# Kernel tuning notes

Hardware: AMD Instinct MI355X
Metric: run time of the kernel (lower is better)

Reference implementation:

```python
import jax, jax.numpy as jnp
import numpy as np

B, S, E, H = 2, 2048, 1024, 16
D = E // H  # head dimension = 64


def setup_inputs() -> dict:
    key = jax.random.key(0)
    ks = jax.random.split(key, 12)
    scale_in = 1.0 / np.sqrt(E)
    x = jax.random.normal(ks[0], (B, S, E), dtype=jnp.float32)
    # random 0/1 attention mask (1 = attend, 0 = masked out)
    mask = jax.random.randint(ks[1], (B, S, S), 0, 2, dtype=jnp.int32)
    # per-head QKV projections, stacked over the head axis: [H, E, D]
    Wq = jax.random.normal(ks[2], (H, E, D), dtype=jnp.float32) * scale_in
    bq = jnp.zeros((H, D), dtype=jnp.float32)
    Wk = jax.random.normal(ks[3], (H, E, D), dtype=jnp.float32) * scale_in
    bk = jnp.zeros((H, D), dtype=jnp.float32)
    Wv = jax.random.normal(ks[4], (H, E, D), dtype=jnp.float32) * scale_in
    bv = jnp.zeros((H, D), dtype=jnp.float32)
    # output projection: [H*D, E] == [E, E]
    Wo = jax.random.normal(ks[5], (H * D, E), dtype=jnp.float32) * scale_in
    bo = jnp.zeros((E,), dtype=jnp.float32)
    return {"x": x, "mask": mask, "Wq": Wq, "bq": bq, "Wk": Wk, "bk": bk,
            "Wv": Wv, "bv": bv, "Wo": Wo, "bo": bo}


def reference(x, mask, Wq, bq, Wk, bk, Wv, bv, Wo, bo):
    # Batched equivalent of the per-head Python loop: all heads at once.
    q = jnp.einsum('bse,hed->bhsd', x, Wq) + bq[None, :, None, :]  # [B,H,S,D]
    k = jnp.einsum('bse,hed->bhsd', x, Wk) + bk[None, :, None, :]
    v = jnp.einsum('bse,hed->bhsd', x, Wv) + bv[None, :, None, :]
    scale = 1.0 / jnp.sqrt(jnp.asarray(D, dtype=q.dtype))
    scores = jnp.einsum('bhsd,bhtd->bhst', q, k) * scale          # [B,H,S,S]
    scores = jnp.where(mask[:, None, :, :] != 0, scores, jnp.asarray(-1e9, scores.dtype))
    attn = jax.nn.softmax(scores, axis=-1)
    ctx = jnp.einsum('bhst,bhtd->bhsd', attn, v)                  # [B,H,S,D]
    # concat heads along feature dim (torch.cat(dim=2))
    concat = jnp.transpose(ctx, (0, 2, 1, 3)).reshape(B, S, H * D)
    return concat @ Wo + bo
```

## Files before the change

kernel.cpp:

```cpp
#include <hip/hip_runtime.h>

#define S_LEN 2048
#define EMB   1024
#define NH    16
#define HD    64
#define BS    2
#define QSCALE 0.18033688f

typedef __bf16 bf16;
typedef bf16  bf16x8 __attribute__((ext_vector_type(8)));
typedef bf16  bf16x4 __attribute__((ext_vector_type(4)));
typedef float f32x4  __attribute__((ext_vector_type(4)));
typedef unsigned long long u64;
typedef unsigned int u32;

__device__ __forceinline__ bf16x8 ld8(const bf16* p){ return *(const bf16x8*)p; }

__device__ __forceinline__ void gl_lds16(const bf16* g, void* l) {
    __builtin_amdgcn_global_load_lds(
        (const __attribute__((address_space(1))) void*)g,
        (__attribute__((address_space(3))) void*)l,
        16, 0, 0);
}

#define SW(row, g) ((((g) ^ ((row) & 7))) * 8)

__global__ __launch_bounds__(256)
void pack_mask(const int* __restrict__ mask, u64* __restrict__ pm)
{
    int lane = threadIdx.x & 63;
    int row  = blockIdx.x * 4 + (threadIdx.x >> 6);
    const int* mr = mask + (size_t)row * S_LEN;
    u64* pr = pm + (size_t)row * (S_LEN / 64);
    for (int i = 0; i < S_LEN / 64; ++i) {
        u64 bits = __ballot(mr[i * 64 + lane] != 0);
        if (lane == 0) pr[i] = bits;
    }
}

__global__ __launch_bounds__(256)
void transpose_w(const float* __restrict__ W0, const float* __restrict__ W1,
                 const float* __restrict__ W2, const float* __restrict__ W3,
                 bf16* __restrict__ Wt)
{
    const int z = blockIdx.z;
    const float* W = z == 0 ? W0 : z == 1 ? W1 : z == 2 ? W2 : W3;
    const bool head = z < 3;
    const int k0 = blockIdx.x * 64, n0 = blockIdx.y * 64;
    const int tid = threadIdx.x;
    __shared__ float T[64][68];
    {
        int k = k0 + (tid >> 2), cg = (tid & 3) * 16;
        size_t base = head ? ((size_t)(n0 >> 6) * ((size_t)EMB * HD) + (size_t)k * HD + cg)
                           : ((size_t)k * EMB + n0 + cg);
        #pragma unroll
        for (int g = 0; g < 4; ++g) {
            f32x4 v = *(const f32x4*)(W + base + g * 4);
            #pragma unroll
            for (int j = 0; j < 4; ++j) T[tid >> 2][cg + g * 4 + j] = v[j];
        }
    }
    __syncthreads();
    {
        int n = n0 + (tid >> 2), ck = (tid & 3) * 16;
        bf16 t16[16];
        #pragma unroll
        for (int j = 0; j < 16; ++j) t16[j] = (bf16)T[ck + j][tid >> 2];
        bf16* outp = Wt + (size_t)z * EMB * EMB + (size_t)n * EMB + k0 + ck;
        *(bf16x8*)outp       = *(bf16x8*)t16;
        *(bf16x8*)(outp + 8) = *(bf16x8*)(t16 + 8);
    }
}

__global__ __launch_bounds__(256)
void cvt_f32_bf16(const float* __restrict__ x, bf16* __restrict__ y)
{
    size_t i = ((size_t)blockIdx.x * 256 + threadIdx.x) * 16;
    bf16 t[16];
    #pragma unroll
    for (int g = 0; g < 4; ++g) {
        f32x4 v = *(const f32x4*)(x + i + g * 4);
        #pragma unroll
        for (int j = 0; j < 4; ++j) t[g * 4 + j] = (bf16)v[j];
    }
    *(bf16x8*)(y + i)     = *(bf16x8*)t;
    *(bf16x8*)(y + i + 8) = *(bf16x8*)(t + 8);
}

__global__ __launch_bounds__(256)
void scale_q(bf16* __restrict__ q)
{
    size_t i = ((size_t)blockIdx.x * 256 + threadIdx.x) * 8;
    bf16x8 v = *(bf16x8*)(q + i);
    #pragma unroll
    for (int j = 0; j < 8; ++j) v[j] = (bf16)((float)v[j] * QSCALE);
    *(bf16x8*)(q + i) = v;
}

__global__ __launch_bounds__(256, 3)
void gemm_qkv(const void* __restrict__ Ap, const bf16* __restrict__ Wt,
              const float* __restrict__ bqp, const float* __restrict__ bkp,
              const float* __restrict__ bvp,
              bf16* __restrict__ qb, bf16* __restrict__ kb, bf16* __restrict__ VT,
              int a32)
{
    const int tid  = threadIdx.x;
    const int lane = tid & 63, quad = lane >> 4, c = lane & 15;
    const int w = tid >> 6, wm = w >> 1, wn = w & 1;
    const int m0 = blockIdx.x * 128;
    const int n0 = blockIdx.y * 128;

    __shared__ bf16 Ash[128][64];
    __shared__ bf16 Wsh[128][64];

    f32x4 acc[4][4];
    #pragma unroll
    for (int mt = 0; mt < 4; ++mt)
        #pragma unroll
        for (int nt = 0; nt < 4; ++nt) acc[mt][nt] = (f32x4){0.f,0.f,0.f,0.f};

    const int lrow = lane >> 3, lcol = (lane & 7) * 8;

    for (int k0 = 0; k0 < EMB; k0 += 64) {
        __syncthreads();
        if (!a32) {
            const bf16* A = (const bf16*)Ap;
            #pragma unroll
            for (int j = 0; j < 4; ++j)
                gl_lds16(A + (size_t)(m0 + w * 32 + j * 8 + lrow) * EMB + k0 + lcol,
                         &Ash[w * 32 + j * 8][0]);
        } else {
            const float* A = (const float*)Ap + (size_t)(m0 + (tid >> 1)) * EMB + k0 + (tid & 1) * 32;
            bf16 t[32];
            #pragma unroll
            for (int g = 0; g < 8; ++g) {
                f32x4 v = *(const f32x4*)(A + g * 4);
                #pragma unroll
                for (int j = 0; j < 4; ++j) t[g * 4 + j] = (bf16)v[j];
            }
            #pragma unroll
            for (int g2 = 0; g2 < 4; ++g2)
                *(bf16x8*)&Ash[tid >> 1][(tid & 1) * 32 + g2 * 8] = *(bf16x8*)(t + g2 * 8);
        }
        #pragma unroll
        for (int j = 0; j < 4; ++j)
            gl_lds16(Wt + (size_t)(n0 + w * 32 + j * 8 + lrow) * EMB + k0 + lcol,
                     &Wsh[w * 32 + j * 8][0]);
        __syncthreads();

        #pragma unroll
        for (int kh = 0; kh < 2; ++kh) {
            bf16x8 af[4], bfv[4];
            #pragma unroll
            for (int mt = 0; mt < 4; ++mt) af[mt]  = ld8(&Ash[wm * 64 + mt * 16 + c][kh * 32 + quad * 8]);
            #pragma unroll
            for (int nt = 0; nt < 4; ++nt) bfv[nt] = ld8(&Wsh[wn * 64 + nt * 16 + c][kh * 32 + quad * 8]);
            #pragma unroll
            for (int mt = 0; mt < 4; ++mt)
                #pragma unroll
                for (int nt = 0; nt < 4; ++nt)
                    acc[mt][nt] = __builtin_amdgcn_mfma_f32_16x16x32_bf16(af[mt], bfv[nt], acc[mt][nt], 0, 0, 0);
        }
    }

    const int z = n0 >> 10;
    const float* bias = z == 0 ? bqp : z == 1 ? bkp : bvp;
    #pragma unroll
    for (int nt = 0; nt < 4; ++nt) {
        int nn = (n0 & 1023) + wn * 64 + nt * 16 + c;
        float bv_ = bias[nn];
        #pragma unroll
        for (int mt = 0; mt < 4; ++mt)
            #pragma unroll
            for (int r = 0; r < 4; ++r) {
                int m = m0 + wm * 64 + mt * 16 + quad * 4 + r;
                float v = acc[mt][nt][r] + bv_;
                if (z == 0)      qb[(size_t)m * EMB + nn] = (bf16)(v * QSCALE);
                else if (z == 1) kb[(size_t)m * EMB + nn] = (bf16)v;
                else {
                    int head = nn >> 6, d = nn & 63;
                    VT[((size_t)((m >> 11) * NH + head) * HD + d) * S_LEN + (m & 2047)] = (bf16)v;
                }
            }
    }
}

__global__ __launch_bounds__(256, 3)
void gemm_o(const bf16* __restrict__ Ap, const bf16* __restrict__ Wt,
            const float* __restrict__ bo, float* __restrict__ C)
{
    const int tid  = threadIdx.x;
    const int lane = tid & 63, quad = lane >> 4, c = lane & 15;
    const int w = tid >> 6, wm = w >> 1, wn = w & 1;
    const int m0 = blockIdx.x * 128;
    const int n0 = blockIdx.y * 128;

    __shared__ bf16 Ash[128][64];
    __shared__ bf16 Wsh[128][64];

    f32x4 acc[4][4];
    #pragma unroll
    for (int mt = 0; mt < 4; ++mt)
        #pragma unroll
        for (int nt = 0; nt < 4; ++nt) acc[mt][nt] = (f32x4){0.f,0.f,0.f,0.f};

    const int lrow = lane >> 3, lcol = (lane & 7) * 8;

    for (int k0 = 0; k0 < EMB; k0 += 64) {
        __syncthreads();
        #pragma unroll
        for (int j = 0; j < 4; ++j)
            gl_lds16(Ap + (size_t)(m0 + w * 32 + j * 8 + lrow) * EMB + k0 + lcol,
                     &Ash[w * 32 + j * 8][0]);
        #pragma unroll
        for (int j = 0; j < 4; ++j)
            gl_lds16(Wt + (size_t)(n0 + w * 32 + j * 8 + lrow) * EMB + k0 + lcol,
                     &Wsh[w * 32 + j * 8][0]);
        __syncthreads();

        #pragma unroll
        for (int kh = 0; kh < 2; ++kh) {
            bf16x8 af[4], bfv[4];
            #pragma unroll
            for (int mt = 0; mt < 4; ++mt) af[mt]  = ld8(&Ash[wm * 64 + mt * 16 + c][kh * 32 + quad * 8]);
            #pragma unroll
            for (int nt = 0; nt < 4; ++nt) bfv[nt] = ld8(&Wsh[wn * 64 + nt * 16 + c][kh * 32 + quad * 8]);
            #pragma unroll
            for (int mt = 0; mt < 4; ++mt)
                #pragma unroll
                for (int nt = 0; nt < 4; ++nt)
                    acc[mt][nt] = __builtin_amdgcn_mfma_f32_16x16x32_bf16(af[mt], bfv[nt], acc[mt][nt], 0, 0, 0);
        }
    }

    #pragma unroll
    for (int nt = 0; nt < 4; ++nt) {
        int n = n0 + wn * 64 + nt * 16 + c;
        float bv_ = bo[n];
        #pragma unroll
        for (int mt = 0; mt < 4; ++mt)
            #pragma unroll
            for (int r = 0; r < 4; ++r) {
                int m = m0 + wm * 64 + mt * 16 + quad * 4 + r;
                C[(size_t)m * EMB + n] = acc[mt][nt][r] + bv_;
            }
    }
}

__global__ __launch_bounds__(512)
void gemm128(const void* __restrict__ Ap, const float* __restrict__ Wp,
             const bf16* __restrict__ Wtp, const float* __restrict__ bias,
             void* __restrict__ Cp, int N, int K, int whead,
             int m_base, int a32, int cmode)
{
    const int tid  = threadIdx.x;
    const int lane = tid & 63, quad = lane >> 4, c = lane & 15;
    const int w = tid >> 6, wm = w >> 2, wn = w & 3;
    const int m0 = blockIdx.x * 128, n0 = blockIdx.y * 128;

    __shared__ bf16 Ash[128][64];
    __shared__ bf16 Wsh[128][64];

    f32x4 acc[4][2];
    #pragma unroll
    for (int mt = 0; mt < 4; ++mt)
        #pragma unroll
        for (int nt = 0; nt < 2; ++nt) acc[mt][nt] = (f32x4){0.f,0.f,0.f,0.f};

    const int arow = tid >> 2, aq = tid & 3;

    auto compute = [&]() {
        #pragma unroll
        for (int kh = 0; kh < 2; ++kh) {
            bf16x8 bfr[2];
            #pragma unroll
            for (int nt = 0; nt < 2; ++nt) {
                int rw = wn * 32 + nt * 16 + c;
                bfr[nt] = ld8(&Wsh[rw][SW(rw, kh * 4 + quad)]);
            }
            #pragma unroll
            for (int mt = 0; mt < 4; ++mt) {
                int ra = wm * 64 + mt * 16 + c;
                bf16x8 af = ld8(&Ash[ra][SW(ra, kh * 4 + quad)]);
                #pragma unroll
                for (int nt = 0; nt < 2; ++nt)
                    acc[mt][nt] = __builtin_amdgcn_mfma_f32_16x16x32_bf16(af, bfr[nt], acc[mt][nt], 0, 0, 0);
            }
        }
    };

    for (int k0 = 0; k0 < K; k0 += 64) {
        __syncthreads();
        if (a32) {
            const float* A = (const float*)Ap + (size_t)(m_base + m0 + arow) * K + k0 + aq * 16;
            bf16 t16[16];
            #pragma unroll
            for (int g = 0; g < 4; ++g) {
                f32x4 v = *(const f32x4*)(A + g * 4);
                #pragma unroll
                for (int j = 0; j < 4; ++j) t16[g * 4 + j] = (bf16)v[j];
            }
            *(bf16x8*)&Ash[arow][SW(arow, aq * 2)]     = *(bf16x8*)t16;
            *(bf16x8*)&Ash[arow][SW(arow, aq * 2 + 1)] = *(bf16x8*)(t16 + 8);
        } else {
            const bf16* A = (const bf16*)Ap + (size_t)(m_base + m0 + arow) * K + k0 + aq * 16;
            *(bf16x8*)&Ash[arow][SW(arow, aq * 2)]     = ld8(A);
            *(bf16x8*)&Ash[arow][SW(arow, aq * 2 + 1)] = ld8(A + 8);
        }
        {
            int nl = tid & 127, kg = tid >> 7;
            int n = n0 + nl;
            size_t base    = whead ? ((size_t)(n >> 6) * ((size_t)K * HD) + (n & 63))
                                   : (size_t)n;
            size_t kstride = whead ? (size_t)HD : (size_t)N;
            #pragma unroll
            for (int p = 0; p < 2; ++p) {
                int grp = kg + 4 * p;
                bf16 t8[8];
                #pragma unroll
                for (int j = 0; j < 8; ++j)
                    t8[j] = (bf16)Wp[base + (size_t)(k0 + grp * 8 + j) * kstride];
                *(bf16x8*)&Wsh[nl][SW(nl, grp)] = *(bf16x8*)t8;
            }
        }
        __syncthreads();
        compute();
    }

    #pragma unroll
    for (int nt = 0; nt < 2; ++nt) {
        int n = n0 + wn * 32 + nt * 16 + c;
        float bv_ = bias[n];
        #pragma unroll
        for (int mt = 0; mt < 4; ++mt)
            #pragma unroll
            for (int r = 0; r < 4; ++r) {
                int m = m0 + wm * 64 + mt * 16 + quad * 4 + r;
                float v = acc[mt][nt][r] + bv_;
                if (cmode == 0)      ((bf16*)Cp)[(size_t)m * N + n] = (bf16)v;
                else if (cmode == 1) ((float*)Cp)[(size_t)m * N + n] = v;
                else {
                    int mm = m_base + m;
                    ((bf16*)Cp)[((size_t)((mm >> 11) * NH + (n >> 6)) * HD + (n & 63)) * S_LEN + (mm & 2047)] = (bf16)v;
                }
            }
    }
}

__global__ __launch_bounds__(512, 2)
void attn_kernel(bf16* q0p, bf16* q1p, const bf16* __restrict__ kbuf,
                 const bf16* __restrict__ VTg, const u64* __restrict__ pmask)
{
    const int tid  = threadIdx.x;
    const int w    = tid >> 6;
    const int lane = tid & 63;
    const int quad = lane >> 4;
    const int c    = lane & 15;
    const int flat  = blockIdx.y * 16 + blockIdx.x;
    const int flat2 = (flat & 7) * 64 + (flat >> 3);
    const int q0   = (flat2 & 15) * 128;
    const int bh   = flat2 >> 4;
    const int b    = bh >> 4, h = bh & 15;

    bf16* qc = b ? q1p : q0p;
    const bf16* kh_ = kbuf + (size_t)b * S_LEN * EMB + h * HD;
    const bf16* vt  = VTg + (size_t)bh * HD * S_LEN;

    __shared__ bf16 Ksh [2][64][64];
    __shared__ bf16 VTsh[2][64][64];
    __shared__ bf16 Psh[8][16][64];

    bf16x8 qf[2];
    #pragma unroll
    for (int kk = 0; kk < 2; ++kk)
        qf[kk] = ld8(qc + (size_t)(q0 + w * 16 + c) * EMB + h * HD + kk * 32 + quad * 8);

    const u64* pmr = pmask + (size_t)(b * S_LEN + q0 + w * 16 + c) * (S_LEN / 64);

    f32x4 l4 = (f32x4){0.f,0.f,0.f,0.f};
    f32x4 o[4];
    #pragma unroll
    for (int dt = 0; dt < 4; ++dt) o[dt] = (f32x4){0.f,0.f,0.f,0.f};

    const int srow = tid >> 3, sg = tid & 7;
    bf16x8 kr, vr;
    auto loadKV = [&](int t0) {
        kr = ld8(kh_ + (size_t)(t0 + srow) * EMB + sg * 8);
        vr = ld8(vt + (size_t)srow * S_LEN + t0 + sg * 8);
    };

    loadKV(0);
    int buf = 0;
    for (int t0 = 0; t0 < S_LEN; t0 += 64) {
        *(bf16x8*)&Ksh [buf][srow][SW(srow, sg)] = kr;
        *(bf16x8*)&VTsh[buf][srow][SW(srow, sg)] = vr;
        __syncthreads();
        if (t0 + 64 < S_LEN) loadKV(t0 + 64);

        u64 s0 = pmr[t0 >> 6] >> (quad * 4);
        u32 mm[2] = {(u32)s0, (u32)(s0 >> 32)};

        f32x4 sc[4];
        #pragma unroll
        for (int tt = 0; tt < 4; ++tt) sc[tt] = (f32x4){0.f,0.f,0.f,0.f};
        #pragma unroll
        for (int tt = 0; tt < 4; ++tt)
            #pragma unroll
            for (int kk = 0; kk < 2; ++kk) {
                int rk = tt * 16 + c;
                bf16x8 ka = ld8(&Ksh[buf][rk][SW(rk, kk * 4 + quad)]);
                sc[tt] = __builtin_amdgcn_mfma_f32_16x16x32_bf16(ka, qf[kk], sc[tt], 0, 0, 0);
            }

        #pragma unroll
        for (int tt = 0; tt < 4; ++tt) {
            u32 half = mm[tt >> 1];
            bf16x4 pv;
            #pragma unroll
            for (int r = 0; r < 4; ++r) {
                float e = __builtin_amdgcn_exp2f(sc[tt][r]);
                e = ((half >> ((tt & 1) * 16 + r)) & 1) ? e : 0.f;
                l4[r] += e;
                pv[r] = (bf16)e;
            }
            *(bf16x4*)&Psh[w][c][SW(c, tt * 2 + (quad >> 1)) + (quad & 1) * 4] = pv;
        }
        __builtin_amdgcn_s_waitcnt(0xc07f);

        #pragma unroll
        for (int th = 0; th < 2; ++th) {
            bf16x8 pf = ld8(&Psh[w][c][SW(c, th * 4 + quad)]);
            #pragma unroll
            for (int dt = 0; dt < 4; ++dt) {
                int rv = dt * 16 + c;
                bf16x8 av = ld8(&VTsh[buf][rv][SW(rv, th * 4 + quad)]);
                o[dt] = __builtin_amdgcn_mfma_f32_16x16x32_bf16(av, pf, o[dt], 0, 0, 0);
            }
        }
        buf ^= 1;
    }

    float ls = l4[0] + l4[1] + l4[2] + l4[3];
    ls += __shfl_xor(ls, 16);
    ls += __shfl_xor(ls, 32);
    float inv = 1.0f / fmaxf(ls, 1e-30f);
    #pragma unroll
    for (int dt = 0; dt < 4; ++dt) {
        bf16x4 ov;
        #pragma unroll
        for (int r = 0; r < 4; ++r) ov[r] = (bf16)(o[dt][r] * inv);
        *(bf16x4*)&qc[(size_t)(q0 + w * 16 + c) * EMB + h * HD + dt * 16 + quad * 4] = ov;
    }
}

extern "C" void kernel_launch(void* const* d_in, const int* in_sizes, int n_in,
                              void* d_out, int out_size, void* d_ws, size_t ws_size,
                              hipStream_t stream)
{
    const float* x    = (const float*)d_in[0];
    const int*   mask = (const int*)d_in[1];
    const float* Wq   = (const float*)d_in[2];
    const float* bq   = (const float*)d_in[3];
    const float* Wk   = (const float*)d_in[4];
    const float* bk   = (const float*)d_in[5];
    const float* Wv   = (const float*)d_in[6];
    const float* bv   = (const float*)d_in[7];
    const float* Wo   = (const float*)d_in[8];
    const float* bo   = (const float*)d_in[9];
    float* out = (float*)d_out;

    const size_t SLAB = (size_t)S_LEN * EMB;
    const size_t QB = (size_t)BS * SLAB * sizeof(bf16);
    const size_t WT = (size_t)4 * EMB * EMB * sizeof(bf16);
    const size_t PM = (size_t)BS * S_LEN * (S_LEN / 64) * 8;
    const size_t XB = (size_t)BS * SLAB * sizeof(bf16);

    bf16* VT = (bf16*)d_out;
    bf16* kb = (bf16*)d_out + BS * SLAB;

    dim3 b256(256), b512(512);
    dim3 gAtt (S_LEN / 128, BS * NH);
    dim3 gT   (EMB / 64, EMB / 64, 4);
    dim3 gPk  (BS * S_LEN / 4);
    dim3 gFull(BS * S_LEN / 128, EMB / 128);
    dim3 gHalf(S_LEN / 128, EMB / 128);

    if (ws_size >= QB + WT + PM + 64) {
        bf16* qb  = (bf16*)d_ws;
        bf16* Wt  = (bf16*)((char*)d_ws + QB);
        u64*  pm  = (u64*)((char*)d_ws + QB + WT);
        const void* xA = x; int a32 = 1;
        if (ws_size >= QB + WT + PM + XB + 64) {
            bf16* xbf = (bf16*)((char*)d_ws + QB + WT + PM);
            cvt_f32_bf16<<<dim3(1024), b256, 0, stream>>>(x, xbf);
            xA = xbf; a32 = 0;
        }
        pack_mask<<<gPk, b256, 0, stream>>>(mask, pm);
        transpose_w<<<gT, b256, 0, stream>>>(Wq, Wk, Wv, Wo, Wt);

        gemm_qkv<<<dim3(BS * S_LEN / 128, 3 * EMB / 128), b256, 0, stream>>>(
            xA, Wt, bq, bk, bv, qb, kb, VT, a32);

        attn_kernel<<<gAtt, b512, 0, stream>>>(qb, qb + SLAB, kb, VT, pm);

        gemm_o<<<dim3(BS * S_LEN / 128, EMB / 128), b256, 0, stream>>>(
            qb, Wt + (size_t)3 * EMB * EMB, bo, out);
    } else if (ws_size >= QB + PM + 64) {
        bf16* qb = (bf16*)d_ws;
        u64*  pm = (u64*)((char*)d_ws + QB);
        pack_mask<<<gPk, b256, 0, stream>>>(mask, pm);

        gemm128<<<gFull, b512, 0, stream>>>(x, Wk, nullptr, bk, kb, EMB, EMB, 1, 0, 1, 0);
        gemm128<<<gFull, b512, 0, stream>>>(x, Wv, nullptr, bv, VT, EMB, EMB, 1, 0, 1, 2);
        gemm128<<<gFull, b512, 0, stream>>>(x, Wq, nullptr, bq, qb, EMB, EMB, 1, 0, 1, 0);
        scale_q<<<dim3(BS * SLAB / (256 * 8)), b256, 0, stream>>>(qb);

        attn_kernel<<<gAtt, b512, 0, stream>>>(qb, qb + SLAB, kb, VT, pm);

        gemm128<<<gFull, b512, 0, stream>>>(qb, Wo, nullptr, bo, out, EMB, EMB, 0, 0, 0, 1);
    } else {
        bf16* qb0 = (bf16*)d_in[4];
        bf16* qb1 = (bf16*)d_in[6];
        u64*  pm  = (u64*)d_in[2];

        gemm128<<<gFull, b512, 0, stream>>>(x, Wk, nullptr, bk, kb, EMB, EMB, 1, 0, 1, 0);
        gemm128<<<gFull, b512, 0, stream>>>(x, Wv, nullptr, bv, VT, EMB, EMB, 1, 0, 1, 2);
        gemm128<<<gHalf, b512, 0, stream>>>(x, Wq, nullptr, bq, qb0, EMB, EMB, 1, 0,     1, 0);
        gemm128<<<gHalf, b512, 0, stream>>>(x, Wq, nullptr, bq, qb1, EMB, EMB, 1, S_LEN, 1, 0);
        scale_q<<<dim3(SLAB / (256 * 8)), b256, 0, stream>>>(qb0);
        scale_q<<<dim3(SLAB / (256 * 8)), b256, 0, stream>>>(qb1);
        pack_mask<<<gPk, b256, 0, stream>>>(mask, pm);

        attn_kernel<<<gAtt, b512, 0, stream>>>(qb0, qb1, kb, VT, pm);

        gemm128<<<gHalf, b512, 0, stream>>>(qb0, Wo, nullptr, bo, out,        EMB, EMB, 0, 0, 0, 1);
        gemm128<<<gHalf, b512, 0, stream>>>(qb1, Wo, nullptr, bo, out + SLAB, EMB, EMB, 0, 0, 0, 1);
    }
}
```

Baseline: 244.1 us.

## Split attention warps 4x2 over query and key/dim halves for operand reuse

Reorganizes the attention kernel's 8 warps into a 4x2 grid. Each warp handles 32 query rows and half of the 64-key tile for QK^T, and half of the head dimension for PV. Each K and V fragment loaded from LDS now feeds two MFMAs, which halves LDS reads per MFMA. In exchange, P is shared through LDS across warps, so each tile needs an extra __syncthreads, and row sums are combined through LDS at the end.

Measured after the change: 245.4 us. Within noise of the previous version (+0.5%).

```diff
diff --git a/kernel.cpp b/kernel.cpp
--- a/kernel.cpp
+++ b/kernel.cpp
@@ -356,6 +356,8 @@
     const int lane = tid & 63;
     const int quad = lane >> 4;
     const int c    = lane & 15;
+    const int qw   = w & 3;
+    const int kw   = w >> 2;
     const int flat  = blockIdx.y * 16 + blockIdx.x;
     const int flat2 = (flat & 7) * 64 + (flat >> 3);
     const int q0   = (flat2 & 15) * 128;
@@ -368,19 +370,25 @@
 
     __shared__ bf16 Ksh [2][64][64];
     __shared__ bf16 VTsh[2][64][64];
-    __shared__ bf16 Psh[8][16][64];
-
-    bf16x8 qf[2];
-    #pragma unroll
-    for (int kk = 0; kk < 2; ++kk)
-        qf[kk] = ld8(qc + (size_t)(q0 + w * 16 + c) * EMB + h * HD + kk * 32 + quad * 8);
-
-    const u64* pmr = pmask + (size_t)(b * S_LEN + q0 + w * 16 + c) * (S_LEN / 64);
-
-    f32x4 l4 = (f32x4){0.f,0.f,0.f,0.f};
-    f32x4 o[4];
-    #pragma unroll
-    for (int dt = 0; dt < 4; ++dt) o[dt] = (f32x4){0.f,0.f,0.f,0.f};
+    __shared__ bf16 Psh[128][64];
+    __shared__ float Lsh[2][4][2][16];
+
+    bf16x8 qf[2][2];
+    #pragma unroll
+    for (int rq = 0; rq < 2; ++rq)
+        #pragma unroll
+        for (int kk = 0; kk < 2; ++kk)
+            qf[rq][kk] = ld8(qc + (size_t)(q0 + qw * 32 + rq * 16 + c) * EMB + h * HD + kk * 32 + quad * 8);
+
+    const u64* pmr0 = pmask + (size_t)(b * S_LEN + q0 + qw * 32 + c) * (S_LEN / 64);
+    const u64* pmr1 = pmr0 + (size_t)16 * (S_LEN / 64);
+
+    float l2[2] = {0.f, 0.f};
+    f32x4 o[2][2];
+    #pragma unroll
+    for (int dt = 0; dt < 2; ++dt)
+        #pragma unroll
+        for (int rq = 0; rq < 2; ++rq) o[dt][rq] = (f32x4){0.f,0.f,0.f,0.f};
 
     const int srow = tid >> 3, sg = tid & 7;
     bf16x8 kr, vr;
@@ -395,61 +403,92 @@
         *(bf16x8*)&Ksh [buf][srow][SW(srow, sg)] = kr;
         *(bf16x8*)&VTsh[buf][srow][SW(srow, sg)] = vr;
         __syncthreads();
+
+        u64 pm0 = pmr0[t0 >> 6], pm1 = pmr1[t0 >> 6];
+        u32 h0 = (u32)(pm0 >> (kw * 32 + quad * 4));
+        u32 h1 = (u32)(pm1 >> (kw * 32 + quad * 4));
+
+        f32x4 sc[2][2];
+        #pragma unroll
+        for (int tt = 0; tt < 2; ++tt)
+            #pragma unroll
+            for (int rq = 0; rq < 2; ++rq) sc[tt][rq] = (f32x4){0.f,0.f,0.f,0.f};
+        #pragma unroll
+        for (int tt = 0; tt < 2; ++tt)
+            #pragma unroll
+            for (int kk = 0; kk < 2; ++kk) {
+                int rk = kw * 32 + tt * 16 + c;
+                bf16x8 ka = ld8(&Ksh[buf][rk][SW(rk, kk * 4 + quad)]);
+                #pragma unroll
+                for (int rq = 0; rq < 2; ++rq)
+                    sc[tt][rq] = __builtin_amdgcn_mfma_f32_16x16x32_bf16(ka, qf[rq][kk], sc[tt][rq], 0, 0, 0);
+            }
+
+        #pragma unroll
+        for (int rq = 0; rq < 2; ++rq) {
+            u32 hh = rq ? h1 : h0;
+            int q = qw * 32 + rq * 16 + c;
+            #pragma unroll
+            for (int tt = 0; tt < 2; ++tt) {
+                bf16x4 pv;
+                #pragma unroll
+                for (int r = 0; r < 4; ++r) {
+                    float e = __builtin_amdgcn_exp2f(sc[tt][rq][r]);
+                    e = ((hh >> (tt * 16 + r)) & 1) ? e : 0.f;
+                    l2[rq] += e;
+                    pv[r] = (bf16)e;
+                }
+                *(bf16x4*)&Psh[q][SW(q, kw * 4 + tt * 2 + (quad >> 1)) + (quad & 1) * 4] = pv;
+            }
+        }
+        __syncthreads();
+
         if (t0 + 64 < S_LEN) loadKV(t0 + 64);
 
-        u64 s0 = pmr[t0 >> 6] >> (quad * 4);
-        u32 mm[2] = {(u32)s0, (u32)(s0 >> 32)};
-
-        f32x4 sc[4];
-        #pragma unroll
-        for (int tt = 0; tt < 4; ++tt) sc[tt] = (f32x4){0.f,0.f,0.f,0.f};
-        #pragma unroll
-        for (int tt = 0; tt < 4; ++tt)
-            #pragma unroll
-            for (int kk = 0; kk < 2; ++kk) {
-                int rk = tt * 16 + c;
-                bf16x8 ka = ld8(&Ksh[buf][rk][SW(rk, kk * 4 + quad)]);
-                sc[tt] = __builtin_amdgcn_mfma_f32_16x16x32_bf16(ka, qf[kk], sc[tt], 0, 0, 0);
-            }
-
-        #pragma unroll
-        for (int tt = 0; tt < 4; ++tt) {
-            u32 half = mm[tt >> 1];
-            bf16x4 pv;
-            #pragma unroll
-            for (int r = 0; r < 4; ++r) {
-                float e = __builtin_amdgcn_exp2f(sc[tt][r]);
-                e = ((half >> ((tt & 1) * 16 + r)) & 1) ? e : 0.f;
-                l4[r] += e;
-                pv[r] = (bf16)e;
-            }
-            *(bf16x4*)&Psh[w][c][SW(c, tt * 2 + (quad >> 1)) + (quad & 1) * 4] = pv;
-        }
-        __builtin_amdgcn_s_waitcnt(0xc07f);
-
         #pragma unroll
         for (int th = 0; th < 2; ++th) {
-            bf16x8 pf = ld8(&Psh[w][c][SW(c, th * 4 + quad)]);
-            #pragma unroll
-            for (int dt = 0; dt < 4; ++dt) {
-                int rv = dt * 16 + c;
+            bf16x8 pf[2];
+            #pragma unroll
+            for (int rq = 0; rq < 2; ++rq) {
+                int q = qw * 32 + rq * 16 + c;
+                pf[rq] = ld8(&Psh[q][SW(q, th * 4 + quad)]);
+            }
+            #pragma unroll
+            for (int dt = 0; dt < 2; ++dt) {
+                int rv = kw * 32 + dt * 16 + c;
                 bf16x8 av = ld8(&VTsh[buf][rv][SW(rv, th * 4 + quad)]);
-                o[dt] = __builtin_amdgcn_mfma_f32_16x16x32_bf16(av, pf, o[dt], 0, 0, 0);
+                #pragma unroll
+                for (int rq = 0; rq < 2; ++rq)
+                    o[dt][rq] = __builtin_amdgcn_mfma_f32_16x16x32_bf16(av, pf[rq], o[dt][rq], 0, 0, 0);
             }
         }
         buf ^= 1;
     }
 
-    float ls = l4[0] + l4[1] + l4[2] + l4[3];
-    ls += __shfl_xor(ls, 16);
-    ls += __shfl_xor(ls, 32);
-    float inv = 1.0f / fmaxf(ls, 1e-30f);
-    #pragma unroll
-    for (int dt = 0; dt < 4; ++dt) {
-        bf16x4 ov;
-        #pragma unroll
-        for (int r = 0; r < 4; ++r) ov[r] = (bf16)(o[dt][r] * inv);
-        *(bf16x4*)&qc[(size_t)(q0 + w * 16 + c) * EMB + h * HD + dt * 16 + quad * 4] = ov;
+    float lr[2];
+    #pragma unroll
+    for (int rq = 0; rq < 2; ++rq) {
+        float t = l2[rq];
+        t += __shfl_xor(t, 16);
+        t += __shfl_xor(t, 32);
+        lr[rq] = t;
+    }
+    if (quad == 0) {
+        Lsh[kw][qw][0][c] = lr[0];
+        Lsh[kw][qw][1][c] = lr[1];
+    }
+    __syncthreads();
+    #pragma unroll
+    for (int rq = 0; rq < 2; ++rq) {
+        float lt = Lsh[0][qw][rq][c] + Lsh[1][qw][rq][c];
+        float inv = 1.0f / fmaxf(lt, 1e-30f);
+        #pragma unroll
+        for (int dt = 0; dt < 2; ++dt) {
+            bf16x4 ov;
+            #pragma unroll
+            for (int r = 0; r < 4; ++r) ov[r] = (bf16)(o[dt][rq][r] * inv);
+            *(bf16x4*)&qc[(size_t)(q0 + qw * 32 + rq * 16 + c) * EMB + h * HD + kw * 32 + dt * 16 + quad * 4] = ov;
+        }
     }
 }
 
```
